# Performance work log

Measured on AMD Instinct MI355X. Metric: run time of the kernel, lower is better.

The kernel has to match this reference:

```python
import jax, jax.numpy as jnp
import numpy as np

N_NODES = 10000
N_EDGES = 160000
D_IN = 512
D_HID = 1024

def setup_inputs() -> dict:
    key = jax.random.key(0)
    ks = jax.random.split(key, 8)
    feat = jax.random.normal(ks[0], (N_NODES, D_IN), dtype=jnp.float32)
    W1 = jax.random.normal(ks[1], (D_IN, D_HID), dtype=jnp.float32) * (1.0 / np.sqrt(D_IN))
    b1 = jnp.zeros((D_HID,), dtype=jnp.float32)
    W2 = jax.random.normal(ks[2], (D_HID, D_IN), dtype=jnp.float32) * (1.0 / np.sqrt(D_HID))
    b2 = jnp.zeros((D_IN,), dtype=jnp.float32)
    eps = jnp.zeros((1,), dtype=jnp.float32)
    src = jax.random.randint(ks[3], (N_EDGES,), 0, N_NODES, dtype=jnp.int32)
    dst = jax.random.randint(ks[4], (N_EDGES,), 0, N_NODES, dtype=jnp.int32)
    return {"feat": feat, "W1": W1, "b1": b1, "W2": W2, "b2": b2,
            "eps": eps, "src": src, "dst": dst}

def reference(feat, W1, b1, W2, b2, eps, src, dst):
    # message passing: copy src feature along each edge, sum-reduce at dst
    msgs = feat[src]                                   # [E, D_IN] gather
    neigh = jax.ops.segment_sum(msgs, dst, num_segments=feat.shape[0])  # [N, D_IN]
    # GIN combine: (1 + eps) * self + sum(neighbors)
    rst = (1.0 + eps[0]) * feat + neigh
    # apply_func: 2-layer MLP with ReLU
    h = jnp.maximum(rst @ W1 + b1, 0.0)
    h = h @ W2 + b2
    # identity residual (in_dim == out_dim)
    return h + feat
```

## Files before the change

### kernel.cpp

```cpp
#include <hip/hip_runtime.h>

typedef unsigned short u16;
typedef unsigned int u32;
typedef __bf16 bf16x8 __attribute__((ext_vector_type(8)));
typedef float f32x4 __attribute__((ext_vector_type(4)));

#define N_NODES 10000
#define N_EDGES 160000
#define D_IN 512
#define D_HID 1024

#define AS1 __attribute__((address_space(1)))
#define AS3 __attribute__((address_space(3)))

__device__ __forceinline__ u16 f2bf(float f) {
    union { float f; u32 u; } v; v.f = f;
    return (u16)((v.u + 0x7fffu + ((v.u >> 16) & 1u)) >> 16);
}
__device__ __forceinline__ float b2f(u32 h) {
    union { u32 u; float f; } v; v.u = h << 16; return v.f;
}

__global__ void hist_k(const int* __restrict__ dst, int* __restrict__ counts) {
    int e = blockIdx.x * 256 + threadIdx.x;
    if (e < N_EDGES) atomicAdd(&counts[dst[e]], 1);
}

__global__ __launch_bounds__(1024) void scan_k(const int* __restrict__ counts,
                                               int* __restrict__ offs,
                                               int* __restrict__ cursor) {
    __shared__ int wpre[16];
    int t = threadIdx.x, l = t & 63, w = t >> 6;
    int base = t * 10;
    int c[10];
    int lsum = 0;
#pragma unroll
    for (int i = 0; i < 10; i++) {
        int idx = base + i;
        c[i] = (idx < N_NODES) ? counts[idx] : 0;
        lsum += c[i];
    }
    int sc = lsum;
#pragma unroll
    for (int d = 1; d < 64; d <<= 1) {
        int v = __shfl_up(sc, d);
        if (l >= d) sc += v;
    }
    __shared__ int wsum[16];
    if (l == 63) wsum[w] = sc;
    __syncthreads();
    if (w == 0 && l < 16) {
        int v = wsum[l];
        int p = v;
#pragma unroll
        for (int d = 1; d < 16; d <<= 1) {
            int u = __shfl_up(p, d);
            if (l >= d) p += u;
        }
        wpre[l] = p - v;
    }
    __syncthreads();
    int run = wpre[w] + sc - lsum;
#pragma unroll
    for (int i = 0; i < 10; i++) {
        int idx = base + i;
        if (idx < N_NODES) { offs[idx] = run; cursor[idx] = run; run += c[i]; }
    }
    if (t == 1023) offs[N_NODES] = wpre[15] + sc;
}

__global__ void reorder_k(const int* __restrict__ src, const int* __restrict__ dst,
                          int* __restrict__ cursor, int* __restrict__ ssrc) {
    int e = blockIdx.x * 256 + threadIdx.x;
    if (e >= N_EDGES) return;
    int d = dst[e];
    int pos = atomicAdd(&cursor[d], 1);
    ssrc[pos] = src[e];
}

__global__ void cvt_bf16_k(const float* __restrict__ in, u16* __restrict__ out, int n) {
    int i = (blockIdx.x * 256 + threadIdx.x) * 8;
    if (i >= n) return;
    float4 a = *(const float4*)(in + i);
    float4 b = *(const float4*)(in + i + 4);
    uint4 o;
    o.x = (u32)f2bf(a.x) | ((u32)f2bf(a.y) << 16);
    o.y = (u32)f2bf(a.z) | ((u32)f2bf(a.w) << 16);
    o.z = (u32)f2bf(b.x) | ((u32)f2bf(b.y) << 16);
    o.w = (u32)f2bf(b.z) | ((u32)f2bf(b.w) << 16);
    *(uint4*)(out + i) = o;
}

__global__ void transw_k(const float* __restrict__ W1, u16* __restrict__ w1t,
                         const float* __restrict__ W2, u16* __restrict__ w2t) {
    __shared__ float tile[32][33];
    int b = blockIdx.x;
    const float* W; u16* WT; int K, N, nt;
    if (b < 512) { W = W1; WT = w1t; K = D_IN;  N = D_HID; nt = 32; }
    else         { b -= 512; W = W2; WT = w2t; K = D_HID; N = D_IN;  nt = 16; }
    int n0 = (b % nt) * 32, k0 = (b / nt) * 32;
    int tx = threadIdx.x, ty = threadIdx.y;
#pragma unroll
    for (int i = 0; i < 32; i += 8)
        tile[ty + i][tx] = W[(size_t)(k0 + ty + i) * N + n0 + tx];
    __syncthreads();
#pragma unroll
    for (int i = 0; i < 32; i += 8)
        WT[(size_t)(n0 + ty + i) * K + k0 + tx] = f2bf(tile[tx][ty + i]);
}

__global__ __launch_bounds__(128) void gather_k(const float* __restrict__ feat,
                                                const u16* __restrict__ featb,
                                                const float* __restrict__ eps,
                                                const int* __restrict__ offs,
                                                const int* __restrict__ ssrc,
                                                u16* __restrict__ out) {
    int n = (blockIdx.x * 128 + threadIdx.x) >> 6;
    int l = threadIdx.x & 63;
    if (n >= N_NODES) return;
    int beg = offs[n], end = offs[n + 1];
    float s = 1.0f + eps[0];
    float4 s0 = *(const float4*)(feat + (size_t)n * D_IN + l * 8);
    float4 s1 = *(const float4*)(feat + (size_t)n * D_IN + l * 8 + 4);
    float acc[8] = { s * s0.x, s * s0.y, s * s0.z, s * s0.w,
                     s * s1.x, s * s1.y, s * s1.z, s * s1.w };
    int e = beg;
    for (; e + 4 <= end; e += 4) {
        int i0 = ssrc[e], i1 = ssrc[e + 1], i2 = ssrc[e + 2], i3 = ssrc[e + 3];
        uint4 v0 = *(const uint4*)(featb + (size_t)i0 * D_IN + l * 8);
        uint4 v1 = *(const uint4*)(featb + (size_t)i1 * D_IN + l * 8);
        uint4 v2 = *(const uint4*)(featb + (size_t)i2 * D_IN + l * 8);
        uint4 v3 = *(const uint4*)(featb + (size_t)i3 * D_IN + l * 8);
#define ACC4(v) \
        acc[0] += b2f(v.x & 0xffffu); acc[1] += b2f(v.x >> 16); \
        acc[2] += b2f(v.y & 0xffffu); acc[3] += b2f(v.y >> 16); \
        acc[4] += b2f(v.z & 0xffffu); acc[5] += b2f(v.z >> 16); \
        acc[6] += b2f(v.w & 0xffffu); acc[7] += b2f(v.w >> 16);
        ACC4(v0) ACC4(v1) ACC4(v2) ACC4(v3)
    }
    for (; e < end; e++) {
        int i0 = ssrc[e];
        uint4 v0 = *(const uint4*)(featb + (size_t)i0 * D_IN + l * 8);
        ACC4(v0)
    }
#undef ACC4
    uint4 o;
    o.x = (u32)f2bf(acc[0]) | ((u32)f2bf(acc[1]) << 16);
    o.y = (u32)f2bf(acc[2]) | ((u32)f2bf(acc[3]) << 16);
    o.z = (u32)f2bf(acc[4]) | ((u32)f2bf(acc[5]) << 16);
    o.w = (u32)f2bf(acc[6]) | ((u32)f2bf(acc[7]) << 16);
    *(uint4*)(out + (size_t)n * D_IN + l * 8) = o;
}

template <int EPI>
__global__ __launch_bounds__(256, 2) void gemm_k(const u16* __restrict__ A,
                                                 const u16* __restrict__ BT,
                                                 const float* __restrict__ bias,
                                                 const float* __restrict__ feat,
                                                 void* __restrict__ Cout,
                                                 int M, int N, int K) {
    __shared__ __bf16 sA[4][128 * 32];
    __shared__ __bf16 sB[4][128 * 32];

    const int NX = gridDim.x;
    const int nwg = NX * gridDim.y;
    const int flat = blockIdx.y * NX + blockIdx.x;
    const int qq = nwg >> 3, rr8 = nwg & 7;
    const int xcd = flat & 7, idx = flat >> 3;
    const int L = (xcd < rr8 ? xcd * (qq + 1) : rr8 * (qq + 1) + (xcd - rr8) * qq) + idx;
    const int row0 = (L / NX) * 128;
    const int col0 = (L % NX) * 128;

    const int t = threadIdx.x;
    const int w = t >> 6, l = t & 63;
    const int wm = (w >> 1) * 64, wn = (w & 1) * 64;
    const int lr = l & 15;
    const int lq = l >> 4;

    const u16* pA[2];
    const u16* pB[2];
    int ldo[2];
    {
        int g8 = (((l & 3) ^ ((l >> 3) & 3)) * 8);
        int rl = l >> 2;
#pragma unroll
        for (int h = 0; h < 2; h++) {
            int R = w * 32 + h * 16;
            int ar = row0 + R + rl; if (ar > M - 1) ar = M - 1;
            pA[h] = A + (size_t)ar * K + g8;
            int br = col0 + R + rl;
            pB[h] = BT + (size_t)br * K + g8;
            ldo[h] = R * 32;
        }
    }
    const int fo = ((lq ^ ((lr >> 1) & 3)) * 8);

    f32x4 acc[4][4] = {};
    const int NT = K >> 5;

    auto STAGE = [&](int buf, int kt) {
        const int ko = kt << 5;
#pragma unroll
        for (int h = 0; h < 2; h++) {
            __builtin_amdgcn_global_load_lds((const AS1 void*)(pA[h] + ko),
                                             (AS3 void*)(&sA[buf][ldo[h]]), 16, 0, 0);
            __builtin_amdgcn_global_load_lds((const AS1 void*)(pB[h] + ko),
                                             (AS3 void*)(&sB[buf][ldo[h]]), 16, 0, 0);
        }
    };

    STAGE(0, 0);
    STAGE(1, 1);
    STAGE(2, 2);

    for (int it = 0; it < NT; ++it) {
        asm volatile("s_waitcnt vmcnt(8)" ::: "memory");
        __builtin_amdgcn_sched_barrier(0);
        __builtin_amdgcn_s_barrier();
        int kt = it + 3;
        STAGE((it + 3) & 3, kt < NT ? kt : 0);
        const __bf16* cA = &sA[it & 3][0];
        const __bf16* cB = &sB[it & 3][0];
        bf16x8 fa[4], fb[4];
#pragma unroll
        for (int i = 0; i < 4; i++)
            fa[i] = *(const bf16x8*)(cA + (wm + i * 16 + lr) * 32 + fo);
#pragma unroll
        for (int j = 0; j < 4; j++)
            fb[j] = *(const bf16x8*)(cB + (wn + j * 16 + lr) * 32 + fo);
#pragma unroll
        for (int i = 0; i < 4; i++)
#pragma unroll
            for (int j = 0; j < 4; j++)
                acc[i][j] = __builtin_amdgcn_mfma_f32_16x16x32_bf16(
                    fa[i], fb[j], acc[i][j], 0, 0, 0);
    }

#pragma unroll
    for (int i = 0; i < 4; i++) {
        int rowb = row0 + wm + i * 16 + lq * 4;
#pragma unroll
        for (int j = 0; j < 4; j++) {
            int col = col0 + wn + j * 16 + lr;
            float bv = bias[col];
#pragma unroll
            for (int r = 0; r < 4; r++) {
                int rr = rowb + r;
                if (rr < M) {
                    float v = acc[i][j][r] + bv;
                    if (EPI == 0) {
                        v = fmaxf(v, 0.0f);
                        ((u16*)Cout)[(size_t)rr * N + col] = f2bf(v);
                    } else {
                        v += feat[(size_t)rr * N + col];
                        ((float*)Cout)[(size_t)rr * N + col] = v;
                    }
                }
            }
        }
    }
}

extern "C" void kernel_launch(void* const* d_in, const int* in_sizes, int n_in,
                              void* d_out, int out_size, void* d_ws, size_t ws_size,
                              hipStream_t stream) {
    const float* feat = (const float*)d_in[0];
    const float* W1   = (const float*)d_in[1];
    const float* b1   = (const float*)d_in[2];
    const float* W2   = (const float*)d_in[3];
    const float* b2   = (const float*)d_in[4];
    const float* eps  = (const float*)d_in[5];
    const int*   src  = (const int*)d_in[6];
    const int*   dst  = (const int*)d_in[7];
    float* out = (float*)d_out;

    char* ws = (char*)d_ws;
    u16* rst_b16 = (u16*)(ws);
    u16* h_b16   = (u16*)(ws + 10240000);
    u16* featb   = (u16*)(ws + 30720000);
    u16* w1t     = (u16*)(ws + 40960000);
    u16* w2t     = (u16*)(ws + 42008576);
    int* counts  = (int*)(ws + 43057152);
    int* offs    = (int*)(ws + 43097152);
    int* cursor  = (int*)(ws + 43137160);
    int* ssrc    = (int*)(ws + 43177160);

    const int NE = N_NODES * D_IN;

    hipMemsetAsync(counts, 0, N_NODES * sizeof(int), stream);
    hist_k<<<(N_EDGES + 255) / 256, 256, 0, stream>>>(dst, counts);
    scan_k<<<1, 1024, 0, stream>>>(counts, offs, cursor);
    reorder_k<<<(N_EDGES + 255) / 256, 256, 0, stream>>>(src, dst, cursor, ssrc);

    cvt_bf16_k<<<NE / 8 / 256, 256, 0, stream>>>(feat, featb, NE);
    transw_k<<<1024, dim3(32, 8), 0, stream>>>(W1, w1t, W2, w2t);

    gather_k<<<(N_NODES + 1) / 2, 128, 0, stream>>>(feat, featb, eps, offs, ssrc, rst_b16);

    const int MT = (N_NODES + 127) / 128;
    gemm_k<0><<<dim3(D_HID / 128, MT), 256, 0, stream>>>(rst_b16, w1t, b1, nullptr,
                                                         (void*)h_b16, N_NODES, D_HID, D_IN);
    gemm_k<1><<<dim3(D_IN / 128, MT), 256, 0, stream>>>(h_b16, w2t, b2, feat,
                                                        (void*)out, N_NODES, D_IN, D_HID);
}
```

Measured before the change: 228.9 us.

## Use single-wave 64x64 GEMM tiles with double-buffered BK=64 staging

Replaces the 256-thread 128x128 GEMM tiles (4-stage, BK=32) with 64-thread single-wavefront 64x64 tiles, a 2-stage BK=64 LDS pipeline and compile-time K. With one wave per block the workgroup barrier goes away, and the last row tile is clamped to overlap instead of using bounds checks. The aim is more blocks for the small M=10000 problem and less sync overhead. The cost is less data reuse per tile, more global traffic, and a shallow pipeline that waits on vmcnt(0) each iteration. The overlapping rows in the last tile are recomputed and stored redundantly.

```diff
diff --git a/kernel.cpp b/kernel.cpp
--- a/kernel.cpp
+++ b/kernel.cpp
@@ -152,15 +152,15 @@
     *(uint4*)(out + (size_t)n * D_IN + l * 8) = o;
 }
 
-template <int EPI>
-__global__ __launch_bounds__(256, 2) void gemm_k(const u16* __restrict__ A,
-                                                 const u16* __restrict__ BT,
-                                                 const float* __restrict__ bias,
-                                                 const float* __restrict__ feat,
-                                                 void* __restrict__ Cout,
-                                                 int M, int N, int K) {
-    __shared__ __bf16 sA[4][128 * 32];
-    __shared__ __bf16 sB[4][128 * 32];
+template <int EPI, int K>
+__global__ __launch_bounds__(64) void gemm_k(const u16* __restrict__ A,
+                                             const u16* __restrict__ BT,
+                                             const float* __restrict__ bias,
+                                             const float* __restrict__ feat,
+                                             void* __restrict__ Cout,
+                                             int M, int N) {
+    __shared__ __bf16 sA[2][64 * 64];
+    __shared__ __bf16 sB[2][64 * 64];
 
     const int NX = gridDim.x;
     const int nwg = NX * gridDim.y;
@@ -168,93 +168,92 @@
     const int qq = nwg >> 3, rr8 = nwg & 7;
     const int xcd = flat & 7, idx = flat >> 3;
     const int L = (xcd < rr8 ? xcd * (qq + 1) : rr8 * (qq + 1) + (xcd - rr8) * qq) + idx;
-    const int row0 = (L / NX) * 128;
-    const int col0 = (L % NX) * 128;
-
-    const int t = threadIdx.x;
-    const int w = t >> 6, l = t & 63;
-    const int wm = (w >> 1) * 64, wn = (w & 1) * 64;
+    int row0 = (L / NX) * 64;
+    if (row0 > M - 64) row0 = M - 64;
+    const int col0 = (L % NX) * 64;
+
+    const int l = threadIdx.x;
     const int lr = l & 15;
     const int lq = l >> 4;
 
-    const u16* pA[2];
-    const u16* pB[2];
-    int ldo[2];
-    {
-        int g8 = (((l & 3) ^ ((l >> 3) & 3)) * 8);
-        int rl = l >> 2;
-#pragma unroll
-        for (int h = 0; h < 2; h++) {
-            int R = w * 32 + h * 16;
-            int ar = row0 + R + rl; if (ar > M - 1) ar = M - 1;
-            pA[h] = A + (size_t)ar * K + g8;
-            int br = col0 + R + rl;
-            pB[h] = BT + (size_t)br * K + g8;
-            ldo[h] = R * 32;
-        }
-    }
-    const int fo = ((lq ^ ((lr >> 1) & 3)) * 8);
+    const int g8 = (((l & 7) ^ (l >> 3)) * 8);
+    const u16* bA = A  + (size_t)(row0 + (l >> 3)) * K + g8;
+    const u16* bB = BT + (size_t)(col0 + (l >> 3)) * K + g8;
+    const int fo = ((lq ^ (lr & 7)) * 8);
 
     f32x4 acc[4][4] = {};
-    const int NT = K >> 5;
-
-    auto STAGE = [&](int buf, int kt) {
-        const int ko = kt << 5;
-#pragma unroll
-        for (int h = 0; h < 2; h++) {
-            __builtin_amdgcn_global_load_lds((const AS1 void*)(pA[h] + ko),
-                                             (AS3 void*)(&sA[buf][ldo[h]]), 16, 0, 0);
-            __builtin_amdgcn_global_load_lds((const AS1 void*)(pB[h] + ko),
-                                             (AS3 void*)(&sB[buf][ldo[h]]), 16, 0, 0);
-        }
-    };
+    const int NT = K >> 6;
+
+#define STAGE(buf, kt)                                                         \
+    {                                                                          \
+        const int ko_ = (kt) << 6;                                             \
+        _Pragma("unroll")                                                      \
+        for (int q_ = 0; q_ < 8; q_++) {                                       \
+            __builtin_amdgcn_global_load_lds(                                  \
+                (const AS1 void*)(bA + (size_t)q_ * 8 * K + ko_),              \
+                (AS3 void*)(&sA[buf][q_ * 512]), 16, 0, 0);                    \
+            __builtin_amdgcn_global_load_lds(                                  \
+                (const AS1 void*)(bB + (size_t)q_ * 8 * K + ko_),              \
+                (AS3 void*)(&sB[buf][q_ * 512]), 16, 0, 0);                    \
+        }                                                                      \
+    }
 
     STAGE(0, 0);
-    STAGE(1, 1);
-    STAGE(2, 2);
-
+
+#pragma unroll
     for (int it = 0; it < NT; ++it) {
-        asm volatile("s_waitcnt vmcnt(8)" ::: "memory");
+        const int cur = it & 1;
+        asm volatile("s_waitcnt vmcnt(0)" ::: "memory");
         __builtin_amdgcn_sched_barrier(0);
-        __builtin_amdgcn_s_barrier();
-        int kt = it + 3;
-        STAGE((it + 3) & 3, kt < NT ? kt : 0);
-        const __bf16* cA = &sA[it & 3][0];
-        const __bf16* cB = &sB[it & 3][0];
         bf16x8 fa[4], fb[4];
 #pragma unroll
         for (int i = 0; i < 4; i++)
-            fa[i] = *(const bf16x8*)(cA + (wm + i * 16 + lr) * 32 + fo);
+            fa[i] = *(const bf16x8*)(&sA[cur][0] + (i * 16 + lr) * 64 + (fo ^ 0));
 #pragma unroll
         for (int j = 0; j < 4; j++)
-            fb[j] = *(const bf16x8*)(cB + (wn + j * 16 + lr) * 32 + fo);
+            fb[j] = *(const bf16x8*)(&sB[cur][0] + (j * 16 + lr) * 64 + (fo ^ 0));
+        bf16x8 fa2[4], fb2[4];
+#pragma unroll
+        for (int i = 0; i < 4; i++)
+            fa2[i] = *(const bf16x8*)(&sA[cur][0] + (i * 16 + lr) * 64 + (fo ^ 32));
+#pragma unroll
+        for (int j = 0; j < 4; j++)
+            fb2[j] = *(const bf16x8*)(&sB[cur][0] + (j * 16 + lr) * 64 + (fo ^ 32));
+        __builtin_amdgcn_sched_barrier(0);
+        if (it + 1 < NT) STAGE(cur ^ 1, it + 1);
+        __builtin_amdgcn_sched_barrier(0);
 #pragma unroll
         for (int i = 0; i < 4; i++)
 #pragma unroll
             for (int j = 0; j < 4; j++)
                 acc[i][j] = __builtin_amdgcn_mfma_f32_16x16x32_bf16(
                     fa[i], fb[j], acc[i][j], 0, 0, 0);
-    }
+#pragma unroll
+        for (int i = 0; i < 4; i++)
+#pragma unroll
+            for (int j = 0; j < 4; j++)
+                acc[i][j] = __builtin_amdgcn_mfma_f32_16x16x32_bf16(
+                    fa2[i], fb2[j], acc[i][j], 0, 0, 0);
+    }
+#undef STAGE
 
 #pragma unroll
     for (int i = 0; i < 4; i++) {
-        int rowb = row0 + wm + i * 16 + lq * 4;
+        int rowb = row0 + i * 16 + lq * 4;
 #pragma unroll
         for (int j = 0; j < 4; j++) {
-            int col = col0 + wn + j * 16 + lr;
+            int col = col0 + j * 16 + lr;
             float bv = bias[col];
 #pragma unroll
             for (int r = 0; r < 4; r++) {
                 int rr = rowb + r;
-                if (rr < M) {
-                    float v = acc[i][j][r] + bv;
-                    if (EPI == 0) {
-                        v = fmaxf(v, 0.0f);
-                        ((u16*)Cout)[(size_t)rr * N + col] = f2bf(v);
-                    } else {
-                        v += feat[(size_t)rr * N + col];
-                        ((float*)Cout)[(size_t)rr * N + col] = v;
-                    }
+                float v = acc[i][j][r] + bv;
+                if (EPI == 0) {
+                    v = fmaxf(v, 0.0f);
+                    ((u16*)Cout)[(size_t)rr * N + col] = f2bf(v);
+                } else {
+                    v += feat[(size_t)rr * N + col];
+                    ((float*)Cout)[(size_t)rr * N + col] = v;
                 }
             }
         }
@@ -297,9 +296,9 @@
 
     gather_k<<<(N_NODES + 1) / 2, 128, 0, stream>>>(feat, featb, eps, offs, ssrc, rst_b16);
 
-    const int MT = (N_NODES + 127) / 128;
-    gemm_k<0><<<dim3(D_HID / 128, MT), 256, 0, stream>>>(rst_b16, w1t, b1, nullptr,
-                                                         (void*)h_b16, N_NODES, D_HID, D_IN);
-    gemm_k<1><<<dim3(D_IN / 128, MT), 256, 0, stream>>>(h_b16, w2t, b2, feat,
-                                                        (void*)out, N_NODES, D_IN, D_HID);
-}
+    const int MT = (N_NODES + 63) / 64;
+    gemm_k<0, D_IN><<<dim3(D_HID / 64, MT), 64, 0, stream>>>(
+        rst_b16, w1t, b1, nullptr, (void*)h_b16, N_NODES, D_HID);
+    gemm_k<1, D_HID><<<dim3(D_IN / 64, MT), 64, 0, stream>>>(
+        h_b16, w2t, b2, feat, (void*)out, N_NODES, D_IN);
+}
```

New measurement: 198.9 us. 13.1% less time.
